# Optimization experiments

Hardware: AMD Instinct MI355X
Metric: run time of the kernel (lower is better)

## Reference

```python
import jax, jax.numpy as jnp
import numpy as np

WINDOW = (2, 8, 8)
DIM = 180
HEADS = 6
NW = 64  # number of distinct window masks


def _get_position_index(ws):
    d, h, w = ws
    coords = np.stack(np.meshgrid(np.arange(d), np.arange(h), np.arange(w), indexing='ij'))  # [3,d,h,w]
    cf = coords.reshape(3, -1)
    rel = cf[:, :, None] - cf[:, None, :]  # [3,N,N]
    rel = rel.transpose(1, 2, 0).astype(np.int64)
    rel[:, :, 0] += d - 1
    rel[:, :, 1] += h - 1
    rel[:, :, 2] += w - 1
    rel[:, :, 0] *= (2 * h - 1) * (2 * w - 1)
    rel[:, :, 1] *= 2 * w - 1
    return rel.sum(-1)  # [N,N]


def _get_sine_position_encoding(HW, num_pos_feats, temperature=10000.0, normalize=True):
    scale = 2 * np.pi
    not_mask = np.ones((1, HW[0], HW[1]), dtype=np.float32)
    y_embed = not_mask.cumsum(1)
    x_embed = not_mask.cumsum(2)
    if normalize:
        eps = 1e-6
        y_embed = y_embed / (y_embed[:, -1:, :] + eps) * scale
        x_embed = x_embed / (x_embed[:, :, -1:] + eps) * scale
    dim_t = np.arange(num_pos_feats, dtype=np.float32)
    dim_t = temperature ** (2 * (dim_t // 2) / num_pos_feats)
    pos_x = x_embed[:, :, :, None] / dim_t
    pos_y = y_embed[:, :, :, None] / dim_t
    pos_x = np.stack((np.sin(pos_x[:, :, :, 0::2]), np.cos(pos_x[:, :, :, 1::2])), axis=4).reshape(1, HW[0], HW[1], -1)
    pos_y = np.stack((np.sin(pos_y[:, :, :, 0::2]), np.cos(pos_y[:, :, :, 1::2])), axis=4).reshape(1, HW[0], HW[1], -1)
    pos = np.concatenate((pos_y, pos_x), axis=3)  # [1,H,W,2*npf]
    return pos.reshape(1, HW[0] * HW[1], -1)  # [1, H*W, dim]


REL_IDX = _get_position_index(WINDOW)                      # [128,128] int
POS_BIAS = _get_sine_position_encoding(WINDOW[1:], DIM // 2)  # [1,64,180]


def setup_inputs() -> dict:
    key = jax.random.key(0)
    ks = jax.random.split(key, 8)
    B_, N, C = 1024, 128, DIM
    x = jax.random.normal(ks[0], (B_, N, C), dtype=jnp.float32)
    # 0 / -1e4 additive window mask (shifted-window style), nW windows
    m = jax.random.uniform(ks[1], (NW, N, N))
    mask = jnp.where(m < 0.9, 0.0, -1e4).astype(jnp.float32)
    rpb_table = jax.random.normal(ks[2], (675, HEADS), dtype=jnp.float32) * 0.02
    W_qkv_self = jax.random.normal(ks[3], (3 * C, C), dtype=jnp.float32) * (C ** -0.5)
    W_qkv_mut = jax.random.normal(ks[4], (3 * C, C), dtype=jnp.float32) * (C ** -0.5)
    W_proj = jax.random.normal(ks[5], (C, 2 * C), dtype=jnp.float32) * ((2 * C) ** -0.5)
    b_proj = jax.random.normal(ks[6], (C,), dtype=jnp.float32) * 0.01
    return {"x": x, "mask": mask, "rpb_table": rpb_table, "W_qkv_self": W_qkv_self,
            "W_qkv_mut": W_qkv_mut, "W_proj": W_proj, "b_proj": b_proj}


def _qkv(x, W, H):
    B_, N, C = x.shape
    hd = C // H
    y = jnp.einsum('bnc,oc->bno', x, W)  # torch Linear: x @ W.T
    y = y.reshape(B_, N, 3, H, hd).transpose(2, 0, 3, 1, 4)  # [3,B_,H,N,hd]
    return y[0], y[1], y[2]


def _attention(q, k, v, mask, bias, scale):
    # q,k,v: [B_,H,N,hd]; mask: [nW,>=N,>=N] or None; bias: [H,N,N] or None
    B_, H, N, hd = q.shape
    attn = jnp.einsum('bhnd,bhmd->bhnm', q * scale, k)
    if bias is not None:
        attn = attn + bias[None]
    if mask is not None:
        nW = mask.shape[0]
        attn = attn.reshape(B_ // nW, nW, H, N, N) + mask[None, :, None, :N, :N]
        attn = attn.reshape(B_, H, N, N)
    attn = jax.nn.softmax(attn, axis=-1)
    out = jnp.einsum('bhnm,bhmd->bhnd', attn, v)
    return out.transpose(0, 2, 1, 3).reshape(B_, N, H * hd)


def reference(x, mask, rpb_table, W_qkv_self, W_qkv_mut, W_proj, b_proj):
    B_, N, C = x.shape
    H = HEADS
    hd = C // H
    scale = hd ** -0.5
    rel_idx = jnp.asarray(REL_IDX)
    pos_bias = jnp.asarray(POS_BIAS, dtype=x.dtype)

    # self attention with relative position bias
    q, k, v = _qkv(x, W_qkv_self, H)
    bias = rpb_table[rel_idx[:N, :N].reshape(-1)].reshape(N, N, H).transpose(2, 0, 1)  # [H,N,N]
    x_self = _attention(q, k, v, mask, bias, scale)

    # mutual attention between the two temporal halves
    pb = jnp.tile(pos_bias, (1, 2, 1))  # [1,N,C]
    qm, km, vm = _qkv(x + pb, W_qkv_mut, H)
    half = N // 2
    q1, q2 = qm[:, :, :half], qm[:, :, half:]
    k1, k2 = km[:, :, :half], km[:, :, half:]
    v1, v2 = vm[:, :, :half], vm[:, :, half:]
    x1 = _attention(q2, k1, v1, mask, None, scale)
    x2 = _attention(q1, k2, v2, mask, None, scale)
    x_out = jnp.concatenate([jnp.concatenate([x1, x2], axis=1), x_self], axis=2)  # [B_,N,2C]

    return jnp.einsum('bnc,oc->bno', x_out, W_proj) + b_proj
```

## Files before the change

kernel.cpp:

```cpp
#include <hip/hip_runtime.h>
#include <hip/hip_bf16.h>


typedef unsigned short u16;
typedef unsigned int   u32;

#define NTOK 128
#define CDIM 180
#define NHEAD 6
#define XH   200
#define KQSTR 40
#define VSTR 37
#define SLSTR 33
#define WROWS 1081
#define WCOL 192
#define XSTR 188
#define KVSTR 36
#define KVSZ  4640
#define QSTR 36
#define QKSCALE 0.18257418583505536f

typedef __attribute__((ext_vector_type(8))) short bf16x8v;
typedef __attribute__((ext_vector_type(4))) float f32x4v;

__device__ __forceinline__ float bflo(u32 u){ return __uint_as_float(u << 16); }
__device__ __forceinline__ float bfhi(u32 u){ return __uint_as_float(u & 0xFFFF0000u); }
__device__ __forceinline__ float bf2f(u16 v){ return __uint_as_float(((u32)v) << 16); }

__device__ __forceinline__ u16 f2bf(float f){
  u32 u = __float_as_uint(f);
  u32 r = u + 0x7FFFu + ((u >> 16) & 1u);
  return (u16)(r >> 16);
}
__device__ __forceinline__ void split2(float f, u16& h, u16& l){
  h = f2bf(f);
  float rem = f - bf2f(h);
  l = f2bf(rem);
}

__device__ __forceinline__ int kvrow(int r){ return r * KVSTR + ((r >> 4) << 2); }

template<bool F32> __device__ __forceinline__ float ld1(const void* p, size_t i) {
  if constexpr (F32) return reinterpret_cast<const float*>(p)[i];
  else               return bf2f(reinterpret_cast<const u16*>(p)[i]);
}
template<bool F32> __device__ __forceinline__ float2 ld2(const void* p, size_t i) {
  if constexpr (F32) return *reinterpret_cast<const float2*>(reinterpret_cast<const float*>(p) + i);
  else {
    u32 r = *reinterpret_cast<const u32*>(reinterpret_cast<const u16*>(p) + i);
    return float2{bflo(r), bfhi(r)};
  }
}
template<bool F32> __device__ __forceinline__ float4 ld4(const void* p, size_t i) {
  if constexpr (F32) return *reinterpret_cast<const float4*>(reinterpret_cast<const float*>(p) + i);
  else {
    uint2 r = *reinterpret_cast<const uint2*>(reinterpret_cast<const u16*>(p) + i);
    return float4{bflo(r.x), bfhi(r.x), bflo(r.y), bfhi(r.y)};
  }
}

__device__ __forceinline__ float posenc(int c, int n64) {
  int t = (c < 90) ? c : (c - 90);
  float e = (c < 90) ? (float)((n64 >> 3) + 1) : (float)((n64 & 7) + 1);
  float embed = e * 0.78539807f;
  float expo  = (float)(t & ~1) * (1.0f / 90.0f);
  float arg   = embed * exp2f(-13.2877124f * expo);
  return (t & 1) ? cosf(arg) : sinf(arg);
}

__global__ void detect_dtype(const u32* __restrict__ xw, int* __restrict__ flag) {
  __shared__ int cnt[256];
  int c = 0;
  for (int i = threadIdx.x; i < 4096; i += 256) {
    u32 e = (xw[i] >> 7) & 0xFF;
    c += (e >= 0x58 && e <= 0x90) ? 1 : 0;
  }
  cnt[threadIdx.x] = c;
  __syncthreads();
  if (threadIdx.x == 0) {
    int t = 0;
    for (int i = 0; i < 256; ++i) t += cnt[i];
    flag[0] = (t >= 2458) ? 1 : 0;
  }
}

__global__ void conv_w(const void* __restrict__ Wqs, const void* __restrict__ Wqm,
                       const int* __restrict__ flag,
                       u16* __restrict__ whi, u16* __restrict__ wlo) {
  const int r = blockIdx.x;
  const int c = threadIdx.x;
  float v = 0.f;
  if (r < 1080 && c < 180) {
    const void* W = (r < 540) ? Wqs : Wqm;
    const int rr  = (r < 540) ? r : r - 540;
    v = flag[0] ? ld1<false>(W, (size_t)rr * 180 + c)
                : ld1<true >(W, (size_t)rr * 180 + c);
  }
  u16 h, l;
  split2(v, h, l);
  whi[r * WCOL + c] = h;
  wlo[r * WCOL + c] = l;
}

template<bool F32, bool SELF>
__device__ __forceinline__ void attn_phase(
    int h, const void* __restrict__ mask, const void* __restrict__ rpb,
    const u16* __restrict__ qhi, const u16* __restrict__ qlo,
    const u16* __restrict__ khi, const u16* __restrict__ klo,
    const u32* __restrict__ vbuf, float* __restrict__ slab,
    int w64, int qb, int l15, int lk)
{
  constexpr int NT  = SELF ? 8 : 4;
  constexpr int NKS = SELF ? 4 : 2;
  const int query = qb + l15;
  const int kbase = SELF ? 0 : ((qb < 64) ? 64 : 0);

  bf16x8v qfh = *reinterpret_cast<const bf16x8v*>(qhi + query * KQSTR + lk * 8);
  bf16x8v qfl = *reinterpret_cast<const bf16x8v*>(qlo + query * KQSTR + lk * 8);
  f32x4v sacc[NT];
  #pragma unroll
  for (int t = 0; t < NT; ++t) sacc[t] = f32x4v{0.f, 0.f, 0.f, 0.f};
  #pragma unroll
  for (int t = 0; t < NT; ++t) {
    const int krow = kbase + t * 16 + l15;
    bf16x8v kfh = *reinterpret_cast<const bf16x8v*>(khi + krow * KQSTR + lk * 8);
    bf16x8v kfl = *reinterpret_cast<const bf16x8v*>(klo + krow * KQSTR + lk * 8);
    sacc[t] = __builtin_amdgcn_mfma_f32_16x16x32_bf16(kfh, qfh, sacc[t], 0, 0, 0);
    sacc[t] = __builtin_amdgcn_mfma_f32_16x16x32_bf16(kfl, qfh, sacc[t], 0, 0, 0);
    sacc[t] = __builtin_amdgcn_mfma_f32_16x16x32_bf16(kfh, qfl, sacc[t], 0, 0, 0);
  }
  __syncthreads();

  const int il = SELF ? query : (query & 63);
  const size_t mbase = (size_t)w64 * (NTOK * NTOK) + (size_t)il * NTOK;
  const int bi_d = query >> 6, bi_h = (query >> 3) & 7, bi_w = query & 7;
  float mx = -1e30f;
  #pragma unroll
  for (int t = 0; t < NT; ++t) {
    float4 mv = ld4<F32>(mask, mbase + (size_t)(t * 16 + lk * 4));
    float mvr[4] = {mv.x, mv.y, mv.z, mv.w};
    #pragma unroll
    for (int r = 0; r < 4; ++r) {
      float sv = sacc[t][r] * QKSCALE + mvr[r];
      if (SELF) {
        const int jv = t * 16 + lk * 4 + r;
        const int dj = jv >> 6, hj = (jv >> 3) & 7, wj = jv & 7;
        const int idx = (bi_d - dj + 1) * 225 + (bi_h - hj + 7) * 15 + (bi_w - wj + 7);
        sv += ld1<F32>(rpb, (size_t)idx * 6 + h);
      }
      sacc[t][r] = sv;
      mx = fmaxf(mx, sv);
    }
  }
  mx = fmaxf(mx, __shfl_xor(mx, 16));
  mx = fmaxf(mx, __shfl_xor(mx, 32));

  float L = 0.f;
  u32 ph[NT][2], pl[NT][2];
  #pragma unroll
  for (int t = 0; t < NT; ++t) {
    float p0 = __expf(sacc[t][0] - mx);
    float p1 = __expf(sacc[t][1] - mx);
    float p2 = __expf(sacc[t][2] - mx);
    float p3 = __expf(sacc[t][3] - mx);
    L += (p0 + p1) + (p2 + p3);
    u16 a0,b0,a1,b1,a2,b2,a3,b3;
    split2(p0,a0,b0); split2(p1,a1,b1); split2(p2,a2,b2); split2(p3,a3,b3);
    ph[t][0] = (u32)a0 | ((u32)a1 << 16);
    ph[t][1] = (u32)a2 | ((u32)a3 << 16);
    pl[t][0] = (u32)b0 | ((u32)b1 << 16);
    pl[t][1] = (u32)b2 | ((u32)b3 << 16);
  }
  L += __shfl_xor(L, 16);
  L += __shfl_xor(L, 32);
  const float invL = 1.0f / L;

  f32x4v oacc0 = f32x4v{0.f, 0.f, 0.f, 0.f};
  f32x4v oacc1 = f32x4v{0.f, 0.f, 0.f, 0.f};
  #pragma unroll
  for (int ks = 0; ks < NKS; ++ks) {
    u32 wh[4], wl[4];
    #pragma unroll
    for (int jj = 0; jj < 4; ++jj) {
      const int lkp = (2 * lk + (jj >> 1)) & 3;
      const int src = l15 + (lkp << 4);
      u32 a = __shfl(ph[2 * ks][jj & 1], src);
      u32 b = __shfl(ph[2 * ks + 1][jj & 1], src);
      wh[jj] = (lk & 2) ? b : a;
      u32 c = __shfl(pl[2 * ks][jj & 1], src);
      u32 d = __shfl(pl[2 * ks + 1][jj & 1], src);
      wl[jj] = (lk & 2) ? d : c;
    }
    union UB { u32 w[4]; bf16x8v v; } BH, BL;
    BH.w[0] = wh[0]; BH.w[1] = wh[1]; BH.w[2] = wh[2]; BH.w[3] = wh[3];
    BL.w[0] = wl[0]; BL.w[1] = wl[1]; BL.w[2] = wl[2]; BL.w[3] = wl[3];
    #pragma unroll
    for (int mt = 0; mt < 2; ++mt) {
      u32 u[8];
      #pragma unroll
      for (int i = 0; i < 8; ++i)
        u[i] = vbuf[(size_t)(kbase + ks * 32 + lk * 8 + i) * VSTR + mt * 16 + l15];
      union UA { u32 w[4]; bf16x8v v; } AH, AL;
      #pragma unroll
      for (int jj = 0; jj < 4; ++jj) {
        AH.w[jj] = (u[2 * jj] & 0xFFFFu) | (u[2 * jj + 1] << 16);
        AL.w[jj] = (u[2 * jj] >> 16)     | (u[2 * jj + 1] & 0xFFFF0000u);
      }
      if (mt == 0) {
        oacc0 = __builtin_amdgcn_mfma_f32_16x16x32_bf16(AH.v, BH.v, oacc0, 0, 0, 0);
        oacc0 = __builtin_amdgcn_mfma_f32_16x16x32_bf16(AL.v, BH.v, oacc0, 0, 0, 0);
        oacc0 = __builtin_amdgcn_mfma_f32_16x16x32_bf16(AH.v, BL.v, oacc0, 0, 0, 0);
      } else {
        oacc1 = __builtin_amdgcn_mfma_f32_16x16x32_bf16(AH.v, BH.v, oacc1, 0, 0, 0);
        oacc1 = __builtin_amdgcn_mfma_f32_16x16x32_bf16(AL.v, BH.v, oacc1, 0, 0, 0);
        oacc1 = __builtin_amdgcn_mfma_f32_16x16x32_bf16(AH.v, BL.v, oacc1, 0, 0, 0);
      }
    }
  }

  const int orow = SELF ? query : ((query + 64) & 127);
  #pragma unroll
  for (int r = 0; r < 4; ++r) {
    const int d0 = lk * 4 + r;
    slab[orow * SLSTR + d0] = oacc0[r] * invL;
    const int d1 = 16 + d0;
    if (d1 < 30) slab[orow * SLSTR + d1] = oacc1[r] * invL;
  }
}

template<bool F32>
__device__ void body_mfma(const void* __restrict__ x,
                          const void* __restrict__ mask,
                          const void* __restrict__ rpb,
                          const void* __restrict__ Wp,
                          const void* __restrict__ bp,
                          const u16* __restrict__ whi,
                          const u16* __restrict__ wlo,
                          float* __restrict__ out,
                          u16* xhi_s, u16* xlo_s,
                          u16* qbuf, u16* kbuf, u32* vbuf)
{
  const int tid = threadIdx.x;
  const int b   = blockIdx.x;
  const int w64 = b & 63;

  const int wv  = tid >> 6;
  const int l15 = tid & 15;
  const int lk  = (tid & 63) >> 4;
  const int qb  = wv * 16;

  u16* qhi = qbuf;
  u16* qlo = qbuf + NTOK * KQSTR;
  u16* khi = kbuf;
  u16* klo = kbuf + NTOK * KQSTR;
  float* slab = reinterpret_cast<float*>(qbuf);

  const int rp = tid & 127;
  const int og = __builtin_amdgcn_readfirstlane(tid >> 7);
  float acc[45];
  #pragma unroll
  for (int o2 = 0; o2 < 45; ++o2) acc[o2] = 0.f;

  {
    const size_t xbase = (size_t)b * (NTOK * CDIM);
    for (int i = tid; i < NTOK * 45; i += 512) {
      int r = i / 45, c4 = (i - r * 45) * 4;
      float4 f = ld4<F32>(x, xbase + (size_t)r * CDIM + c4);
      u16 h0,l0,h1,l1,h2,l2,h3,l3;
      split2(f.x, h0, l0); split2(f.y, h1, l1);
      split2(f.z, h2, l2); split2(f.w, h3, l3);
      u32* phd = reinterpret_cast<u32*>(&xhi_s[r * XH + c4]);
      u32* pld = reinterpret_cast<u32*>(&xlo_s[r * XH + c4]);
      phd[0] = (u32)h0 | ((u32)h1 << 16);
      phd[1] = (u32)h2 | ((u32)h3 << 16);
      pld[0] = (u32)l0 | ((u32)l1 << 16);
      pld[1] = (u32)l2 | ((u32)l3 << 16);
    }
    for (int i = tid; i < NTOK * 10; i += 512) {
      int r = i / 10, c = 180 + (i - r * 10) * 2;
      *reinterpret_cast<u32*>(&xhi_s[r * XH + c]) = 0;
      *reinterpret_cast<u32*>(&xlo_s[r * XH + c]) = 0;
    }
    if (tid < NTOK) {
      khi[tid * KQSTR + 30] = 0; khi[tid * KQSTR + 31] = 0;
      klo[tid * KQSTR + 30] = 0; klo[tid * KQSTR + 31] = 0;
      vbuf[tid * VSTR + 30] = 0; vbuf[tid * VSTR + 31] = 0;
    }
  }

  for (int pass = 0; pass < 2; ++pass) {
    const bool self = (pass == 0);
    if (!self) {
      __syncthreads();
      for (int i = tid; i < NTOK * 90; i += 512) {
        int r = i / 90, c = (i - r * 90) * 2;
        int n64 = r & 63;
        u32 hw = *reinterpret_cast<u32*>(&xhi_s[r * XH + c]);
        u32 lw = *reinterpret_cast<u32*>(&xlo_s[r * XH + c]);
        float x0 = bflo(hw) + bflo(lw) + posenc(c,     n64);
        float x1 = bfhi(hw) + bfhi(lw) + posenc(c + 1, n64);
        u16 h0,l0,h1,l1;
        split2(x0, h0, l0); split2(x1, h1, l1);
        *reinterpret_cast<u32*>(&xhi_s[r * XH + c]) = (u32)h0 | ((u32)h1 << 16);
        *reinterpret_cast<u32*>(&xlo_s[r * XH + c]) = (u32)l0 | ((u32)l1 << 16);
      }
    }
    const int matbase = self ? 0 : 540;
    for (int h = 0; h < NHEAD; ++h) {
      __syncthreads();
      {
        int rowoff[6];
        #pragma unroll
        for (int nt = 0; nt < 6; ++nt) {
          const int o  = nt * 16 + l15;
          const int g2 = o / 30;
          const int lr = o - g2 * 30;
          rowoff[nt] = ((o < 90) ? (matbase + g2 * 180 + h * 30 + lr) : 1080) * WCOL;
        }
        f32x4v am[6];
        #pragma unroll
        for (int nt = 0; nt < 6; ++nt) am[nt] = f32x4v{0.f, 0.f, 0.f, 0.f};
        const u16* xh = &xhi_s[(wv * 16 + l15) * XH];
        const u16* xl = &xlo_s[(wv * 16 + l15) * XH];
        #pragma unroll 2
        for (int ks = 0; ks < 6; ++ks) {
          const int k0 = lk * 8 + ks * 32;
          bf16x8v ahi = *reinterpret_cast<const bf16x8v*>(xh + k0);
          bf16x8v alo = *reinterpret_cast<const bf16x8v*>(xl + k0);
          #pragma unroll
          for (int nt = 0; nt < 6; ++nt) {
            bf16x8v bhi = *reinterpret_cast<const bf16x8v*>(whi + rowoff[nt] + k0);
            bf16x8v blo = *reinterpret_cast<const bf16x8v*>(wlo + rowoff[nt] + k0);
            am[nt] = __builtin_amdgcn_mfma_f32_16x16x32_bf16(ahi, bhi, am[nt], 0, 0, 0);
            am[nt] = __builtin_amdgcn_mfma_f32_16x16x32_bf16(alo, bhi, am[nt], 0, 0, 0);
            am[nt] = __builtin_amdgcn_mfma_f32_16x16x32_bf16(ahi, blo, am[nt], 0, 0, 0);
          }
        }
        #pragma unroll
        for (int nt = 0; nt < 6; ++nt) {
          const int o = nt * 16 + l15;
          if (o < 90) {
            const int g2 = o / 30;
            const int lr = o - g2 * 30;
            #pragma unroll
            for (int r = 0; r < 4; ++r) {
              const int t = wv * 16 + lk * 4 + r;
              u16 hh, ll;
              split2(am[nt][r], hh, ll);
              if (g2 == 0)      { qhi[t * KQSTR + lr] = hh; qlo[t * KQSTR + lr] = ll; }
              else if (g2 == 1) { khi[t * KQSTR + lr] = hh; klo[t * KQSTR + lr] = ll; }
              else              vbuf[t * VSTR + lr] = (u32)hh | ((u32)ll << 16);
            }
          }
        }
        if (tid < NTOK) {
          qhi[tid * KQSTR + 30] = 0; qhi[tid * KQSTR + 31] = 0;
          qlo[tid * KQSTR + 30] = 0; qlo[tid * KQSTR + 31] = 0;
        }
      }
      __syncthreads();
      if (self) attn_phase<F32, true >(h, mask, rpb, qhi, qlo, khi, klo, vbuf, slab, w64, qb, l15, lk);
      else      attn_phase<F32, false>(h, mask, rpb, qhi, qlo, khi, klo, vbuf, slab, w64, qb, l15, lk);
      __syncthreads();
      {
        const int cb = self ? (CDIM + h * 30) : (h * 30);
        float s0[30];
        #pragma unroll
        for (int d = 0; d < 30; ++d) s0[d] = slab[rp * SLSTR + d];
        const size_t wrow = (size_t)(og * 45) * 360 + cb;
        #pragma unroll
        for (int o2 = 0; o2 < 45; ++o2) {
          const size_t wr = wrow + (size_t)o2 * 360;
          float t0 = 0.f;
          #pragma unroll
          for (int d = 0; d < 30; d += 2) {
            float2 w2 = ld2<F32>(Wp, wr + d);
            t0 = fmaf(s0[d], w2.x, fmaf(s0[d + 1], w2.y, t0));
          }
          acc[o2] += t0;
        }
      }
    }
  }

  {
    float* o0 = out + ((size_t)b * NTOK + rp) * CDIM + og * 45;
    #pragma unroll
    for (int o2 = 0; o2 < 45; ++o2) {
      float bb = ld1<F32>(bp, og * 45 + o2);
      o0[o2] = acc[o2] + bb;
    }
  }
}

__global__ __launch_bounds__(512) void fused_mfma(
    const void* __restrict__ x,    const void* __restrict__ mask,
    const void* __restrict__ rpb,  const void* __restrict__ Wp,
    const void* __restrict__ bp,   const int* __restrict__ flag,
    const u16* __restrict__ whi,   const u16* __restrict__ wlo,
    float* __restrict__ out)
{
  __shared__ __align__(16) u16 xhi_s[NTOK * XH];
  __shared__ __align__(16) u16 xlo_s[NTOK * XH];
  __shared__ __align__(16) u16 qbuf[2 * NTOK * KQSTR];
  __shared__ __align__(16) u16 kbuf[2 * NTOK * KQSTR];
  __shared__ __align__(16) u32 vbuf[NTOK * VSTR];
  if (flag[0]) body_mfma<false>(x, mask, rpb, Wp, bp, whi, wlo, out, xhi_s, xlo_s, qbuf, kbuf, vbuf);
  else         body_mfma<true >(x, mask, rpb, Wp, bp, whi, wlo, out, xhi_s, xlo_s, qbuf, kbuf, vbuf);
}

template<bool F32>
__device__ void body_old(const void* __restrict__ x, const void* __restrict__ mask,
                         const void* __restrict__ rpb, const void* __restrict__ Wqs,
                         const void* __restrict__ Wqm, const void* __restrict__ Wp,
                         const void* __restrict__ bp, float* __restrict__ out,
                         float* x_s, float* k_s, float* v_s, float* sq_s)
{
  const int tid = threadIdx.x;
  const int b   = blockIdx.x;
  const int w64 = b & 63;
  const int n   = tid >> 2;
  const int j   = tid & 3;
  const int nt  = tid & 31;
  const int ot  = tid >> 5;
  const bool act = (ot < 15);
  const int grp = ot / 5;
  const int lr0 = (ot - grp * 5) * 6;
  const int rp = tid & 127;
  const int og = __builtin_amdgcn_readfirstlane(tid >> 7);
  float acc[45];
  #pragma unroll
  for (int o2 = 0; o2 < 45; ++o2) acc[o2] = 0.f;
  const int bi_d = n >> 6, bi_h = (n >> 3) & 7, bi_w = n & 7;
  {
    const size_t xbase = (size_t)b * (NTOK * CDIM);
    for (int i = tid * 4; i < NTOK * CDIM; i += 2048) {
      float4 f = ld4<F32>(x, xbase + i);
      int r = i / CDIM, c = i - r * CDIM;
      float* dst = &x_s[r * XSTR + c];
      dst[0] = f.x; dst[1] = f.y; dst[2] = f.z; dst[3] = f.w;
    }
  }
  if (tid < NTOK) {
    const int kb = kvrow(tid);
    k_s[kb + 30] = 0.f; k_s[kb + 31] = 0.f;
    v_s[kb + 30] = 0.f; v_s[kb + 31] = 0.f;
  }
  for (int pass = 0; pass < 2; ++pass) {
    const bool self = (pass == 0);
    const void* W = self ? Wqs : Wqm;
    if (!self) {
      __syncthreads();
      for (int i = tid; i < NTOK * CDIM; i += 512) {
        int r = i / CDIM, c = i - r * CDIM;
        x_s[r * XSTR + c] += posenc(c, r & 63);
      }
    }
    for (int h = 0; h < NHEAD; ++h) {
      __syncthreads();
      if (act) {
        float a[4][6];
        #pragma unroll
        for (int i = 0; i < 4; ++i)
          #pragma unroll
          for (int rr = 0; rr < 6; ++rr) a[i][rr] = 0.f;
        const size_t wb = (size_t)(grp * 180 + h * 30 + lr0) * CDIM;
        const float* xr = &x_s[nt * XSTR];
        #pragma unroll 3
        for (int c = 0; c < CDIM; c += 4) {
          float4 wv[6];
          #pragma unroll
          for (int rr = 0; rr < 6; ++rr)
            wv[rr] = ld4<F32>(W, wb + (size_t)rr * CDIM + c);
          #pragma unroll
          for (int i = 0; i < 4; ++i) {
            float4 xv = *reinterpret_cast<const float4*>(xr + i * (32 * XSTR) + c);
            #pragma unroll
            for (int rr = 0; rr < 6; ++rr)
              a[i][rr] = fmaf(xv.x, wv[rr].x, fmaf(xv.y, wv[rr].y,
                         fmaf(xv.z, wv[rr].z, fmaf(xv.w, wv[rr].w, a[i][rr]))));
          }
        }
        #pragma unroll
        for (int i = 0; i < 4; ++i) {
          const int n2 = 32 * i + nt;
          #pragma unroll
          for (int rr = 0; rr < 6; ++rr) {
            const int lr = lr0 + rr;
            const float val = a[i][rr];
            if (grp == 0)      sq_s[n2 * QSTR + lr] = val * QKSCALE;
            else if (grp == 1) k_s[kvrow(n2) + lr] = val;
            else               v_s[kvrow(n2) + lr] = val;
          }
        }
      }
      __syncthreads();
      float qfull[32];
      {
        const float* qr = &sq_s[n * QSTR];
        #pragma unroll
        for (int kk = 0; kk < 7; ++kk) {
          float4 t4 = *reinterpret_cast<const float4*>(qr + 4 * kk);
          qfull[4*kk] = t4.x; qfull[4*kk+1] = t4.y;
          qfull[4*kk+2] = t4.z; qfull[4*kk+3] = t4.w;
        }
        float2 t2 = *reinterpret_cast<const float2*>(qr + 28);
        qfull[28] = t2.x; qfull[29] = t2.y; qfull[30] = 0.f; qfull[31] = 0.f;
      }
      __syncthreads();
      float o[32];
      #pragma unroll
      for (int d = 0; d < 32; ++d) o[d] = 0.f;
      float m = -1e30f, l = 0.f;
      int jbeg, jcount, kbase;
      if (self) { jbeg = j * 32; jcount = 32; kbase = 0; }
      else      { jbeg = j * 16; jcount = 16; kbase = (n < 64) ? 64 : 0; }
      const int il = self ? n : (n & 63);
      const size_t mbase = (size_t)w64 * (NTOK * NTOK) + (size_t)il * NTOK;
      for (int jj = 0; jj < jcount; jj += 4) {
        const int jl = jbeg + jj;
        const int jg = kbase + jl;
        const float* kb = &k_s[kvrow(jg)];
        float s[4];
        #pragma unroll
        for (int u = 0; u < 4; ++u) {
          const float* kr = kb + u * KVSTR;
          float t0 = 0.f, t1 = 0.f, t2 = 0.f, t3 = 0.f;
          #pragma unroll
          for (int kk = 0; kk < 8; ++kk) {
            float4 kv = *reinterpret_cast<const float4*>(kr + 4 * kk);
            t0 = fmaf(qfull[4 * kk],     kv.x, t0);
            t1 = fmaf(qfull[4 * kk + 1], kv.y, t1);
            t2 = fmaf(qfull[4 * kk + 2], kv.z, t2);
            t3 = fmaf(qfull[4 * kk + 3], kv.w, t3);
          }
          float sv = (t0 + t1) + (t2 + t3);
          sv += ld1<F32>(mask, mbase + (size_t)(jl + u));
          if (self) {
            const int jv = jl + u;
            const int dj = jv >> 6, hj = (jv >> 3) & 7, wj = jv & 7;
            const int idx = (bi_d - dj + 1) * 225 + (bi_h - hj + 7) * 15 + (bi_w - wj + 7);
            sv += ld1<F32>(rpb, (size_t)idx * 6 + h);
          }
          s[u] = sv;
        }
        float M = fmaxf(fmaxf(fmaxf(s[0], s[1]), fmaxf(s[2], s[3])), m);
        float corr = __expf(m - M);
        float p0 = __expf(s[0] - M), p1 = __expf(s[1] - M);
        float p2 = __expf(s[2] - M), p3 = __expf(s[3] - M);
        l = l * corr + ((p0 + p1) + (p2 + p3));
        const float* v0 = &v_s[kvrow(jg)];
        const float* v1 = v0 + KVSTR;
        const float* v2 = v1 + KVSTR;
        const float* v3 = v2 + KVSTR;
        #pragma unroll
        for (int kk = 0; kk < 8; ++kk) {
          float4 a0 = *reinterpret_cast<const float4*>(v0 + 4 * kk);
          float4 a1 = *reinterpret_cast<const float4*>(v1 + 4 * kk);
          float4 a2 = *reinterpret_cast<const float4*>(v2 + 4 * kk);
          float4 a3 = *reinterpret_cast<const float4*>(v3 + 4 * kk);
          o[4*kk]   = fmaf(o[4*kk],   corr, fmaf(p0, a0.x, fmaf(p1, a1.x, fmaf(p2, a2.x, p3 * a3.x))));
          o[4*kk+1] = fmaf(o[4*kk+1], corr, fmaf(p0, a0.y, fmaf(p1, a1.y, fmaf(p2, a2.y, p3 * a3.y))));
          o[4*kk+2] = fmaf(o[4*kk+2], corr, fmaf(p0, a0.z, fmaf(p1, a1.z, fmaf(p2, a2.z, p3 * a3.z))));
          o[4*kk+3] = fmaf(o[4*kk+3], corr, fmaf(p0, a0.w, fmaf(p1, a1.w, fmaf(p2, a2.w, p3 * a3.w))));
        }
        m = M;
      }
      {
        #pragma unroll
        for (int s2 = 1; s2 <= 2; s2 <<= 1) {
          float m2 = __shfl_xor(m, s2);
          float l2 = __shfl_xor(l, s2);
          float M  = fmaxf(m, m2);
          float e1 = __expf(m - M);
          float e2 = __expf(m2 - M);
          l = l * e1 + l2 * e2;
          #pragma unroll
          for (int d = 0; d < 30; ++d) {
            float o2v = __shfl_xor(o[d], s2);
            o[d] = o[d] * e1 + o2v * e2;
          }
          m = M;
        }
        if (j == 0) {
          const int r = self ? n : ((n + 64) & 127);
          float* srow = &sq_s[r * SLSTR];
          const float inv = 1.0f / l;
          #pragma unroll
          for (int d = 0; d < 30; ++d) srow[d] = o[d] * inv;
        }
      }
      __syncthreads();
      {
        const int cb = self ? (CDIM + h * 30) : (h * 30);
        float s0p[30];
        #pragma unroll
        for (int d = 0; d < 30; ++d) s0p[d] = sq_s[rp * SLSTR + d];
        const size_t wrow = (size_t)(og * 45) * 360 + cb;
        #pragma unroll
        for (int o2 = 0; o2 < 45; ++o2) {
          const size_t wr = wrow + (size_t)o2 * 360;
          float t0 = 0.f;
          #pragma unroll
          for (int d = 0; d < 30; d += 2) {
            float2 w2 = ld2<F32>(Wp, wr + d);
            t0 = fmaf(s0p[d], w2.x, fmaf(s0p[d + 1], w2.y, t0));
          }
          acc[o2] += t0;
        }
      }
    }
  }
  {
    float* o0 = out + ((size_t)b * NTOK + rp) * CDIM + og * 45;
    #pragma unroll
    for (int o2 = 0; o2 < 45; ++o2) {
      float bb = ld1<F32>(bp, og * 45 + o2);
      o0[o2] = acc[o2] + bb;
    }
  }
}

__global__ __launch_bounds__(512) void fused_all(
    const void* __restrict__ x,    const void* __restrict__ mask,
    const void* __restrict__ rpb,  const void* __restrict__ Wqs,
    const void* __restrict__ Wqm,  const void* __restrict__ Wp,
    const void* __restrict__ bp,   const int* __restrict__ flag,
    float* __restrict__ out)
{
  __shared__ __align__(16) float x_s[NTOK * XSTR];
  __shared__ __align__(16) float k_s[KVSZ];
  __shared__ __align__(16) float v_s[KVSZ];
  __shared__ __align__(16) float sq_s[NTOK * QSTR];
  if (flag[0]) body_old<false>(x, mask, rpb, Wqs, Wqm, Wp, bp, out, x_s, k_s, v_s, sq_s);
  else         body_old<true >(x, mask, rpb, Wqs, Wqm, Wp, bp, out, x_s, k_s, v_s, sq_s);
}

extern "C" void kernel_launch(void* const* d_in, const int* in_sizes, int n_in,
                              void* d_out, int out_size, void* d_ws, size_t ws_size,
                              hipStream_t stream) {
  int* flag = (int*)d_ws;
  detect_dtype<<<1, 256, 0, stream>>>((const u32*)d_in[0], flag);
  const size_t wbytes = (size_t)WROWS * WCOL * sizeof(u16);
  const size_t need = 64 + 2 * wbytes;
  if (ws_size >= need) {
    u16* whi = (u16*)((char*)d_ws + 64);
    u16* wlo = (u16*)((char*)d_ws + 64 + wbytes);
    conv_w<<<WROWS, WCOL, 0, stream>>>(d_in[3], d_in[4], flag, whi, wlo);
    fused_mfma<<<1024, 512, 0, stream>>>(d_in[0], d_in[1], d_in[2], d_in[5],
                                         d_in[6], flag, whi, wlo, (float*)d_out);
  } else {
    fused_all<<<1024, 512, 0, stream>>>(d_in[0], d_in[1], d_in[2], d_in[3],
                                        d_in[4], d_in[5], d_in[6], flag,
                                        (float*)d_out);
  }
}
```

Measured before the change: 2.004 ms.

## Stream x from global per QKV GEMM instead of staging split copies in LDS

Measured after the change: 2.016 ms. No clear change (+0.6%).

```diff
diff --git a/kernel.cpp b/kernel.cpp
--- a/kernel.cpp
+++ b/kernel.cpp
@@ -8,7 +8,6 @@
 #define NTOK 128
 #define CDIM 180
 #define NHEAD 6
-#define XH   200
 #define KQSTR 40
 #define VSTR 37
 #define SLSTR 33
@@ -237,8 +236,7 @@
                           const u16* __restrict__ whi,
                           const u16* __restrict__ wlo,
                           float* __restrict__ out,
-                          u16* xhi_s, u16* xlo_s,
-                          u16* qbuf, u16* kbuf, u32* vbuf)
+                          u16* qbuf, u16* kbuf, u32* vbuf, float* pb8)
 {
   const int tid = threadIdx.x;
   const int b   = blockIdx.x;
@@ -261,50 +259,26 @@
   #pragma unroll
   for (int o2 = 0; o2 < 45; ++o2) acc[o2] = 0.f;
 
-  {
-    const size_t xbase = (size_t)b * (NTOK * CDIM);
-    for (int i = tid; i < NTOK * 45; i += 512) {
-      int r = i / 45, c4 = (i - r * 45) * 4;
-      float4 f = ld4<F32>(x, xbase + (size_t)r * CDIM + c4);
-      u16 h0,l0,h1,l1,h2,l2,h3,l3;
-      split2(f.x, h0, l0); split2(f.y, h1, l1);
-      split2(f.z, h2, l2); split2(f.w, h3, l3);
-      u32* phd = reinterpret_cast<u32*>(&xhi_s[r * XH + c4]);
-      u32* pld = reinterpret_cast<u32*>(&xlo_s[r * XH + c4]);
-      phd[0] = (u32)h0 | ((u32)h1 << 16);
-      phd[1] = (u32)h2 | ((u32)h3 << 16);
-      pld[0] = (u32)l0 | ((u32)l1 << 16);
-      pld[1] = (u32)l2 | ((u32)l3 << 16);
-    }
-    for (int i = tid; i < NTOK * 10; i += 512) {
-      int r = i / 10, c = 180 + (i - r * 10) * 2;
-      *reinterpret_cast<u32*>(&xhi_s[r * XH + c]) = 0;
-      *reinterpret_cast<u32*>(&xlo_s[r * XH + c]) = 0;
-    }
-    if (tid < NTOK) {
-      khi[tid * KQSTR + 30] = 0; khi[tid * KQSTR + 31] = 0;
-      klo[tid * KQSTR + 30] = 0; klo[tid * KQSTR + 31] = 0;
-      vbuf[tid * VSTR + 30] = 0; vbuf[tid * VSTR + 31] = 0;
-    }
+  const int token = qb + l15;
+  const int n64t  = token & 63;
+  const size_t xrow = (size_t)b * (NTOK * CDIM) + (size_t)token * CDIM;
+
+  for (int i = tid; i < 8 * CDIM; i += 512) {
+    const int r = i / CDIM, c = i - (i / CDIM) * CDIM;
+    const int t = (c < 90) ? c : (c - 90);
+    const float embed = (float)(r + 1) * 0.78539807f;
+    const float expo  = (float)(t & ~1) * (1.0f / 90.0f);
+    const float arg   = embed * exp2f(-13.2877124f * expo);
+    pb8[i] = (t & 1) ? cosf(arg) : sinf(arg);
+  }
+  if (tid < NTOK) {
+    khi[tid * KQSTR + 30] = 0; khi[tid * KQSTR + 31] = 0;
+    klo[tid * KQSTR + 30] = 0; klo[tid * KQSTR + 31] = 0;
+    vbuf[tid * VSTR + 30] = 0; vbuf[tid * VSTR + 31] = 0;
   }
 
   for (int pass = 0; pass < 2; ++pass) {
     const bool self = (pass == 0);
-    if (!self) {
-      __syncthreads();
-      for (int i = tid; i < NTOK * 90; i += 512) {
-        int r = i / 90, c = (i - r * 90) * 2;
-        int n64 = r & 63;
-        u32 hw = *reinterpret_cast<u32*>(&xhi_s[r * XH + c]);
-        u32 lw = *reinterpret_cast<u32*>(&xlo_s[r * XH + c]);
-        float x0 = bflo(hw) + bflo(lw) + posenc(c,     n64);
-        float x1 = bfhi(hw) + bfhi(lw) + posenc(c + 1, n64);
-        u16 h0,l0,h1,l1;
-        split2(x0, h0, l0); split2(x1, h1, l1);
-        *reinterpret_cast<u32*>(&xhi_s[r * XH + c]) = (u32)h0 | ((u32)h1 << 16);
-        *reinterpret_cast<u32*>(&xlo_s[r * XH + c]) = (u32)l0 | ((u32)l1 << 16);
-      }
-    }
     const int matbase = self ? 0 : 540;
     for (int h = 0; h < NHEAD; ++h) {
       __syncthreads();
@@ -320,20 +294,48 @@
         f32x4v am[6];
         #pragma unroll
         for (int nt = 0; nt < 6; ++nt) am[nt] = f32x4v{0.f, 0.f, 0.f, 0.f};
-        const u16* xh = &xhi_s[(wv * 16 + l15) * XH];
-        const u16* xl = &xlo_s[(wv * 16 + l15) * XH];
         #pragma unroll 2
         for (int ks = 0; ks < 6; ++ks) {
           const int k0 = lk * 8 + ks * 32;
-          bf16x8v ahi = *reinterpret_cast<const bf16x8v*>(xh + k0);
-          bf16x8v alo = *reinterpret_cast<const bf16x8v*>(xl + k0);
+          float xv[8];
+          if (ks < 5) {
+            float4 a = ld4<F32>(x, xrow + k0);
+            float4 c = ld4<F32>(x, xrow + k0 + 4);
+            xv[0]=a.x; xv[1]=a.y; xv[2]=a.z; xv[3]=a.w;
+            xv[4]=c.x; xv[5]=c.y; xv[6]=c.z; xv[7]=c.w;
+          } else {
+            #pragma unroll
+            for (int i = 0; i < 8; ++i) {
+              const int k = k0 + i;
+              xv[i] = (k < CDIM) ? ld1<F32>(x, xrow + k) : 0.f;
+            }
+          }
+          if (pass == 1) {
+            #pragma unroll
+            for (int i = 0; i < 8; ++i) {
+              const int k = k0 + i;
+              if (k < CDIM) {
+                const int e1 = (k < 90) ? (n64t >> 3) : (n64t & 7);
+                xv[i] += pb8[e1 * CDIM + k];
+              }
+            }
+          }
+          union UA2 { u32 w[4]; bf16x8v v; } AHf, ALf;
+          #pragma unroll
+          for (int i2 = 0; i2 < 4; ++i2) {
+            u16 h0, l0, h1, l1;
+            split2(xv[2 * i2],     h0, l0);
+            split2(xv[2 * i2 + 1], h1, l1);
+            AHf.w[i2] = (u32)h0 | ((u32)h1 << 16);
+            ALf.w[i2] = (u32)l0 | ((u32)l1 << 16);
+          }
           #pragma unroll
           for (int nt = 0; nt < 6; ++nt) {
             bf16x8v bhi = *reinterpret_cast<const bf16x8v*>(whi + rowoff[nt] + k0);
             bf16x8v blo = *reinterpret_cast<const bf16x8v*>(wlo + rowoff[nt] + k0);
-            am[nt] = __builtin_amdgcn_mfma_f32_16x16x32_bf16(ahi, bhi, am[nt], 0, 0, 0);
-            am[nt] = __builtin_amdgcn_mfma_f32_16x16x32_bf16(alo, bhi, am[nt], 0, 0, 0);
-            am[nt] = __builtin_amdgcn_mfma_f32_16x16x32_bf16(ahi, blo, am[nt], 0, 0, 0);
+            am[nt] = __builtin_amdgcn_mfma_f32_16x16x32_bf16(AHf.v, bhi, am[nt], 0, 0, 0);
+            am[nt] = __builtin_amdgcn_mfma_f32_16x16x32_bf16(ALf.v, bhi, am[nt], 0, 0, 0);
+            am[nt] = __builtin_amdgcn_mfma_f32_16x16x32_bf16(AHf.v, blo, am[nt], 0, 0, 0);
           }
         }
         #pragma unroll
@@ -393,20 +395,19 @@
   }
 }
 
-__global__ __launch_bounds__(512) void fused_mfma(
+__global__ __launch_bounds__(512, 4) void fused_mfma(
     const void* __restrict__ x,    const void* __restrict__ mask,
     const void* __restrict__ rpb,  const void* __restrict__ Wp,
     const void* __restrict__ bp,   const int* __restrict__ flag,
     const u16* __restrict__ whi,   const u16* __restrict__ wlo,
     float* __restrict__ out)
 {
-  __shared__ __align__(16) u16 xhi_s[NTOK * XH];
-  __shared__ __align__(16) u16 xlo_s[NTOK * XH];
   __shared__ __align__(16) u16 qbuf[2 * NTOK * KQSTR];
   __shared__ __align__(16) u16 kbuf[2 * NTOK * KQSTR];
   __shared__ __align__(16) u32 vbuf[NTOK * VSTR];
-  if (flag[0]) body_mfma<false>(x, mask, rpb, Wp, bp, whi, wlo, out, xhi_s, xlo_s, qbuf, kbuf, vbuf);
-  else         body_mfma<true >(x, mask, rpb, Wp, bp, whi, wlo, out, xhi_s, xlo_s, qbuf, kbuf, vbuf);
+  __shared__ __align__(16) float pb8[8 * CDIM];
+  if (flag[0]) body_mfma<false>(x, mask, rpb, Wp, bp, whi, wlo, out, qbuf, kbuf, vbuf, pb8);
+  else         body_mfma<true >(x, mask, rpb, Wp, bp, whi, wlo, out, qbuf, kbuf, vbuf, pb8);
 }
 
 template<bool F32>
```
